# Optimization experiments

Measured on AMD Instinct MI355X. Metric: run time of the kernel, lower is better.

The kernel has to match this reference:

```python
import jax, jax.numpy as jnp
import numpy as np

B, N, C = 4, 4096, 128  # batch, tokens (flattened 3D volume), channels
F = 128  # filters


def setup_inputs() -> dict:
    key = jax.random.key(0)
    ks = jax.random.split(key, 7)
    s = 1.0 / np.sqrt(C)
    return {
        "inputs": jax.random.normal(ks[0], (B, N, C), dtype=jnp.float32),
        "Wq": jax.random.normal(ks[1], (C, F), dtype=jnp.float32) * s,
        "bq": jnp.zeros((F,), dtype=jnp.float32),
        "Wk": jax.random.normal(ks[2], (C, F), dtype=jnp.float32) * s,
        "bk": jnp.zeros((F,), dtype=jnp.float32),
        "Wv": jax.random.normal(ks[3], (C, F), dtype=jnp.float32) * s,
        "bv": jnp.zeros((F,), dtype=jnp.float32),
    }


def reference(inputs, Wq, bq, Wk, bk, Wv, bv):
    # Dense projections
    q = inputs @ Wq + bq  # [B, N, F]
    k = inputs @ Wk + bk
    v = inputs @ Wv + bv
    scale = jnp.sqrt(jnp.asarray(F, dtype=q.dtype))
    scores = jnp.einsum("bnf,bmf->bnm", q, k) / scale  # [B, N, N]
    weights = jax.nn.softmax(scores, axis=-1)
    return jnp.einsum("bnm,bmf->bnf", weights, v)
```

## Files before the change

### kernel.cpp

```cpp
#include <hip/hip_runtime.h>

typedef unsigned short u16;
typedef unsigned int u32;
typedef float f32x4 __attribute__((ext_vector_type(4)));
typedef short s16x8 __attribute__((ext_vector_type(8)));
typedef unsigned int u32x2 __attribute__((ext_vector_type(2)));
typedef unsigned int u32x4 __attribute__((ext_vector_type(4)));

#define NB 4
#define NT 4096
#define ND 128
#define NQ (NB * NT)

#define QK_SCALE 0.12751879523138906f

using as3_void = __attribute__((address_space(3))) void;
using as1_void = __attribute__((address_space(1))) void;

__device__ __forceinline__ u16 f2bf(float x){
  unsigned u = __float_as_uint(x);
  return (u16)((u + 0x7FFFu + ((u >> 16) & 1u)) >> 16);
}
__device__ __forceinline__ u32 cvtpk(float lo, float hi){
  u32 r; asm("v_cvt_pk_bf16_f32 %0, %1, %2" : "=v"(r) : "v"(lo), "v"(hi)); return r;
}
__device__ __forceinline__ f32x4 mfma16(s16x8 a, s16x8 b, f32x4 c){
  return __builtin_amdgcn_mfma_f32_16x16x32_bf16(a, b, c, 0, 0, 0);
}

__global__ void k_wprep(const float* __restrict__ Wq, const float* __restrict__ Wk,
                        const float* __restrict__ Wv, u16* __restrict__ WT){
  int mat = blockIdx.x >> 7;
  int f   = blockIdx.x & 127;
  const float* W = (mat == 0) ? Wq : (mat == 1) ? Wk : Wv;
  int c = threadIdx.x;
  WT[mat * 16384 + f * 128 + c] = f2bf(W[c * 128 + f]);
}

__global__ __launch_bounds__(256) void k_proj(
    const float* __restrict__ X, const u16* __restrict__ WT,
    const float* __restrict__ bq, const float* __restrict__ bk, const float* __restrict__ bv,
    u16* __restrict__ Qs, u16* __restrict__ Ks, u16* __restrict__ VTs)
{
  __shared__ u16 vt[128 * 64];
  const int lane = threadIdx.x & 63;
  const int w    = threadIdx.x >> 6;
  const int lm = lane & 15, lg = lane >> 4;
  const int L   = (blockIdx.x & 7) * 96 + (blockIdx.x >> 3);
  const int mat = L % 3;
  const int rb  = L / 3;
  const int rowbase = rb * 64 + w * 16;

  s16x8 a[4];
  const float* xr = X + (size_t)(rowbase + lm) * ND;
  #pragma unroll
  for (int kc = 0; kc < 4; ++kc){
    f32x4 x0 = *(const f32x4*)(xr + kc * 32 + lg * 8);
    f32x4 x1 = *(const f32x4*)(xr + kc * 32 + lg * 8 + 4);
    s16x8 t;
    t[0]=(short)f2bf(x0[0]); t[1]=(short)f2bf(x0[1]); t[2]=(short)f2bf(x0[2]); t[3]=(short)f2bf(x0[3]);
    t[4]=(short)f2bf(x1[0]); t[5]=(short)f2bf(x1[1]); t[6]=(short)f2bf(x1[2]); t[7]=(short)f2bf(x1[3]);
    a[kc] = t;
  }

  const float* bias = (mat == 0) ? bq : (mat == 1) ? bk : bv;
  float bl[8];
  #pragma unroll
  for (int n = 0; n < 8; ++n) bl[n] = bias[n * 16 + lm];
  f32x4 acc[8];
  #pragma unroll
  for (int n = 0; n < 8; ++n) acc[n] = f32x4{0.f,0.f,0.f,0.f};
  #pragma unroll
  for (int kc = 0; kc < 4; ++kc){
    #pragma unroll
    for (int n = 0; n < 8; ++n){
      s16x8 bf = *(const s16x8*)&WT[mat*16384 + (n*16 + lm)*128 + kc*32 + lg*8];
      acc[n] = mfma16(a[kc], bf, acc[n]);
    }
  }

  if (mat == 0){
    #pragma unroll
    for (int n = 0; n < 8; ++n){
      int f = n * 16 + lm;
      #pragma unroll
      for (int i = 0; i < 4; ++i){
        int r = rowbase + lg * 4 + i;
        Qs[(size_t)r * ND + f] = f2bf((acc[n][i] + bl[n]) * QK_SCALE);
      }
    }
  } else if (mat == 1){
    #pragma unroll
    for (int n = 0; n < 8; ++n){
      int f = n * 16 + lm;
      #pragma unroll
      for (int i = 0; i < 4; ++i){
        int r = rowbase + lg * 4 + i;
        Ks[(size_t)r * ND + (f ^ ((r & 7) << 3))] = f2bf(acc[n][i] + bl[n]);
      }
    }
  } else {
    #pragma unroll
    for (int n = 0; n < 8; ++n){
      int f = n * 16 + lm;
      #pragma unroll
      for (int i = 0; i < 4; ++i){
        int stcol = (w * 16 + lg * 4 + i) ^ ((f & 3) << 3) ^ (((f >> 2) & 1) << 2);
        vt[f * 64 + (stcol ^ ((f & 7) << 3))] = f2bf(acc[n][i] + bl[n]);
      }
    }
    __syncthreads();
    const int b2  = (rb * 64) >> 12;
    const int nt0 = (rb * 64) & (NT - 1);
    #pragma unroll
    for (int it = 0; it < 4; ++it){
      int c = it * 256 + threadIdx.x;
      int f = c >> 3, ch = c & 7;
      s16x8 v = *(const s16x8*)&vt[f * 64 + ((ch * 8) ^ ((f & 7) << 3))];
      *(s16x8*)&VTs[((size_t)b2 * ND + f) * NT + nt0 + ch * 8] = v;
    }
  }
}

__global__ __launch_bounds__(256, 4) void k_attn(
    const u16* __restrict__ Qs, const u16* __restrict__ Ks,
    const u16* __restrict__ VTs, u16* __restrict__ Op, float* __restrict__ lp)
{
  __shared__ __align__(16) u16 kbuf[2][32 * 128];
  __shared__ __align__(16) u16 vbuf[2][128 * 32];

  const int lin = blockIdx.x;
  const int qblk   = (lin & 7) * 16 + (lin >> 6);
  const int eighth = (lin >> 3) & 7;

  const int lane = threadIdx.x & 63;
  const int qw = threadIdx.x >> 6;
  const int lm = lane & 15, lg = lane >> 4;
  const int q0 = qblk * 128 + qw * 32;
  const int b  = q0 >> 12;
  const int kv0 = eighth * 512;

  s16x8 aq[2][4];
  #pragma unroll
  for (int sq = 0; sq < 2; ++sq){
    const u16* qr = Qs + (size_t)(q0 + sq * 16 + lm) * ND;
    #pragma unroll
    for (int kc = 0; kc < 4; ++kc) aq[sq][kc] = *(const s16x8*)(qr + kc * 32 + lg * 8);
  }

  f32x4 o[2][8];
  #pragma unroll
  for (int sq = 0; sq < 2; ++sq)
    #pragma unroll
    for (int n = 0; n < 8; ++n) o[sq][n] = f32x4{0.f,0.f,0.f,0.f};
  float l_[2] = {0.f, 0.f};

  const u16* gk = Ks  + ((size_t)b * NT + kv0 + qw * 8 + (lane >> 4)) * ND + (lane & 15) * 8;
  const u16* gv = VTs + ((size_t)b * ND + qw * 32 + (lane >> 2)) * NT + kv0 + (lane & 3) * 8;

  auto stage = [&](int buf){
    u16* kd = &kbuf[buf][qw * 1024];
    u16* vd = &vbuf[buf][qw * 1024];
    __builtin_amdgcn_global_load_lds((const as1_void*)gk,
                                     (as3_void*)kd, 16, 0, 0);
    __builtin_amdgcn_global_load_lds((const as1_void*)(gk + (size_t)4 * ND),
                                     (as3_void*)(kd + 512), 16, 0, 0);
    __builtin_amdgcn_global_load_lds((const as1_void*)gv,
                                     (as3_void*)vd, 16, 0, 0);
    __builtin_amdgcn_global_load_lds((const as1_void*)(gv + (size_t)16 * NT),
                                     (as3_void*)(vd + 512), 16, 0, 0);
    gk += (size_t)32 * ND;
    gv += 32;
  };

  const int kswz = (lm & 7) << 3;
  const int vswz = ((lm & 3) << 3) ^ (((lm >> 2) & 1) << 2);
  const int vcol0 = (lg * 4) ^ vswz;
  const int vcol1 = (16 + lg * 4) ^ vswz;

  stage(0);
  __syncthreads();
  int par = 0;

  for (int t = 0; t < 16; ++t){
    if (t < 15) stage(par ^ 1);
    const u16* kb = &kbuf[par][0];
    const u16* vb = &vbuf[par][0];

    f32x4 st[2][2];
    #pragma unroll
    for (int sq = 0; sq < 2; ++sq)
      #pragma unroll
      for (int n = 0; n < 2; ++n) st[sq][n] = f32x4{0.f,0.f,0.f,0.f};
    __builtin_amdgcn_s_setprio(1);
    #pragma unroll
    for (int kc = 0; kc < 4; ++kc){
      #pragma unroll
      for (int n = 0; n < 2; ++n){
        s16x8 kf = *(const s16x8*)&kb[(n * 16 + lm) * 128 + ((kc * 32 + lg * 8) ^ kswz)];
        st[0][n] = mfma16(kf, aq[0][kc], st[0][n]);
        st[1][n] = mfma16(kf, aq[1][kc], st[1][n]);
      }
    }
    __builtin_amdgcn_s_setprio(0);

    s16x8 pa[2];
    #pragma unroll
    for (int sq = 0; sq < 2; ++sq){
      float p[8];
      #pragma unroll
      for (int n = 0; n < 2; ++n)
        #pragma unroll
        for (int i = 0; i < 4; ++i){
          p[n * 4 + i] = __builtin_amdgcn_exp2f(st[sq][n][i]);
          l_[sq] += p[n * 4 + i];
        }
      pa[sq] = __builtin_bit_cast(s16x8, u32x4{
          cvtpk(p[0], p[1]), cvtpk(p[2], p[3]),
          cvtpk(p[4], p[5]), cvtpk(p[6], p[7])});
    }

    __builtin_amdgcn_s_setprio(1);
    #pragma unroll
    for (int nf = 0; nf < 8; ++nf){
      const int vr = (nf * 16 + lm) * 32;
      u32x2 v0 = *(const u32x2*)&vb[vr + vcol0];
      u32x2 v1 = *(const u32x2*)&vb[vr + vcol1];
      s16x8 vf = __builtin_bit_cast(s16x8, u32x4{v0[0], v0[1], v1[0], v1[1]});
      o[0][nf] = mfma16(pa[0], vf, o[0][nf]);
      o[1][nf] = mfma16(pa[1], vf, o[1][nf]);
    }
    __builtin_amdgcn_s_setprio(0);

    __syncthreads();
    par ^= 1;
  }

  #pragma unroll
  for (int sq = 0; sq < 2; ++sq){
    float v = l_[sq];
    v += __shfl_xor(v, 16);
    v += __shfl_xor(v, 32);
    l_[sq] = v;
  }
  #pragma unroll
  for (int sq = 0; sq < 2; ++sq){
    #pragma unroll
    for (int i = 0; i < 4; ++i){
      const size_t r = (size_t)eighth * NQ + q0 + sq * 16 + lg * 4 + i;
      #pragma unroll
      for (int nf = 0; nf < 8; ++nf)
        Op[r * ND + nf * 16 + lm] = f2bf(o[sq][nf][i]);
    }
    if (lg == 0) lp[(size_t)eighth * NQ + q0 + sq * 16 + lm] = l_[sq];
  }
}

__global__ __launch_bounds__(256) void k_merge(const u16* __restrict__ Op,
                                               const float* __restrict__ lp,
                                               float* __restrict__ Out){
  const int gid = blockIdx.x * 256 + threadIdx.x;
  const int q = gid >> 4, c = gid & 15;
  float lsum = 0.f;
  #pragma unroll
  for (int e = 0; e < 8; ++e) lsum += lp[(size_t)e * NQ + q];
  const float inv = 1.f / lsum;
  float acc[8] = {0,0,0,0,0,0,0,0};
  #pragma unroll
  for (int e = 0; e < 8; ++e){
    s16x8 v = *(const s16x8*)(Op + ((size_t)e * NQ + q) * ND + c * 8);
    #pragma unroll
    for (int j = 0; j < 8; ++j)
      acc[j] += __uint_as_float(((u32)(u16)v[j]) << 16);
  }
  f32x4 r0{acc[0]*inv, acc[1]*inv, acc[2]*inv, acc[3]*inv};
  f32x4 r1{acc[4]*inv, acc[5]*inv, acc[6]*inv, acc[7]*inv};
  *(f32x4*)(Out + (size_t)q * ND + c * 8)     = r0;
  *(f32x4*)(Out + (size_t)q * ND + c * 8 + 4) = r1;
}

extern "C" void kernel_launch(void* const* d_in, const int* in_sizes, int n_in,
                              void* d_out, int out_size, void* d_ws, size_t ws_size,
                              hipStream_t stream) {
  const float* X  = (const float*)d_in[0];
  const float* Wq = (const float*)d_in[1];
  const float* bq = (const float*)d_in[2];
  const float* Wk = (const float*)d_in[3];
  const float* bk = (const float*)d_in[4];
  const float* Wv = (const float*)d_in[5];
  const float* bv = (const float*)d_in[6];
  float* Out = (float*)d_out;

  u16* Qs  = (u16*)d_ws;
  u16* Ks  = Qs  + (size_t)NQ * ND;
  u16* VTs = Ks  + (size_t)NQ * ND;
  u16* WT  = VTs + (size_t)NQ * ND;
  u16* Op  = WT + 3 * 128 * 128;
  float* lp = (float*)(Op + (size_t)8 * NQ * ND);

  hipLaunchKernelGGL(k_wprep, dim3(3 * 128), dim3(128), 0, stream, Wq, Wk, Wv, WT);
  hipLaunchKernelGGL(k_proj,  dim3(768), dim3(256), 0, stream,
                     X, WT, bq, bk, bv, Qs, Ks, VTs);
  hipLaunchKernelGGL(k_attn,  dim3(1024), dim3(256), 0, stream, Qs, Ks, VTs, Op, lp);
  hipLaunchKernelGGL(k_merge, dim3(NQ * 16 / 256), dim3(256), 0, stream, Op, lp, Out);
}
```

Baseline: 81.87 us.

## Triple-buffer K/V staging with split loads and explicit waitcnt barriers

Replaces the double-buffered K/V LDS pipeline in the attention kernel with a three-stage ring. K and V tiles are now issued separately, two tiles ahead, and each wait uses explicit vmcnt/lgkmcnt counters with raw s_barrier instead of __syncthreads. K and V fragments are loaded into registers before each MFMA phase so LDS reads are grouped away from the matrix ops. This costs 50% more LDS and a lower launch-bounds occupancy hint (3 instead of 4), and adds more barriers per iteration.

```diff
diff --git a/kernel.cpp b/kernel.cpp
--- a/kernel.cpp
+++ b/kernel.cpp
@@ -122,12 +122,12 @@
   }
 }
 
-__global__ __launch_bounds__(256, 4) void k_attn(
+__global__ __launch_bounds__(256, 3) void k_attn(
     const u16* __restrict__ Qs, const u16* __restrict__ Ks,
     const u16* __restrict__ VTs, u16* __restrict__ Op, float* __restrict__ lp)
 {
-  __shared__ __align__(16) u16 kbuf[2][32 * 128];
-  __shared__ __align__(16) u16 vbuf[2][128 * 32];
+  __shared__ __align__(16) u16 kbuf[3][32 * 128];
+  __shared__ __align__(16) u16 vbuf[3][128 * 32];
 
   const int lin = blockIdx.x;
   const int qblk   = (lin & 7) * 16 + (lin >> 6);
@@ -158,18 +158,18 @@
   const u16* gk = Ks  + ((size_t)b * NT + kv0 + qw * 8 + (lane >> 4)) * ND + (lane & 15) * 8;
   const u16* gv = VTs + ((size_t)b * ND + qw * 32 + (lane >> 2)) * NT + kv0 + (lane & 3) * 8;
 
-  auto stage = [&](int buf){
+  auto stageK = [&](int buf){
     u16* kd = &kbuf[buf][qw * 1024];
-    u16* vd = &vbuf[buf][qw * 1024];
-    __builtin_amdgcn_global_load_lds((const as1_void*)gk,
-                                     (as3_void*)kd, 16, 0, 0);
+    __builtin_amdgcn_global_load_lds((const as1_void*)gk, (as3_void*)kd, 16, 0, 0);
     __builtin_amdgcn_global_load_lds((const as1_void*)(gk + (size_t)4 * ND),
                                      (as3_void*)(kd + 512), 16, 0, 0);
-    __builtin_amdgcn_global_load_lds((const as1_void*)gv,
-                                     (as3_void*)vd, 16, 0, 0);
+    gk += (size_t)32 * ND;
+  };
+  auto stageV = [&](int buf){
+    u16* vd = &vbuf[buf][qw * 1024];
+    __builtin_amdgcn_global_load_lds((const as1_void*)gv, (as3_void*)vd, 16, 0, 0);
     __builtin_amdgcn_global_load_lds((const as1_void*)(gv + (size_t)16 * NT),
                                      (as3_void*)(vd + 512), 16, 0, 0);
-    gk += (size_t)32 * ND;
     gv += 32;
   };
 
@@ -178,15 +178,30 @@
   const int vcol0 = (lg * 4) ^ vswz;
   const int vcol1 = (16 + lg * 4) ^ vswz;
 
-  stage(0);
-  __syncthreads();
-  int par = 0;
+  stageK(0); stageV(0); stageK(1); stageV(1);
+
+  int r = 0, s = 2;
 
   for (int t = 0; t < 16; ++t){
-    if (t < 15) stage(par ^ 1);
-    const u16* kb = &kbuf[par][0];
-    const u16* vb = &vbuf[par][0];
-
+    if (t < 15) asm volatile("s_waitcnt vmcnt(4)" ::: "memory");
+    else        asm volatile("s_waitcnt vmcnt(0)" ::: "memory");
+    __builtin_amdgcn_sched_barrier(0);
+    __builtin_amdgcn_s_barrier();
+    __builtin_amdgcn_sched_barrier(0);
+
+    const u16* kb = &kbuf[r][0];
+    const u16* vb = &vbuf[r][0];
+
+    s16x8 kf[2][4];
+    #pragma unroll
+    for (int kc = 0; kc < 4; ++kc){
+      kf[0][kc] = *(const s16x8*)&kb[lm * 128        + ((kc * 32 + lg * 8) ^ kswz)];
+      kf[1][kc] = *(const s16x8*)&kb[(16 + lm) * 128 + ((kc * 32 + lg * 8) ^ kswz)];
+    }
+    if (t < 14) stageK(s);
+    __builtin_amdgcn_s_barrier();
+    asm volatile("s_waitcnt lgkmcnt(0)" ::: "memory");
+    __builtin_amdgcn_sched_barrier(0);
     f32x4 st[2][2];
     #pragma unroll
     for (int sq = 0; sq < 2; ++sq)
@@ -197,12 +212,12 @@
     for (int kc = 0; kc < 4; ++kc){
       #pragma unroll
       for (int n = 0; n < 2; ++n){
-        s16x8 kf = *(const s16x8*)&kb[(n * 16 + lm) * 128 + ((kc * 32 + lg * 8) ^ kswz)];
-        st[0][n] = mfma16(kf, aq[0][kc], st[0][n]);
-        st[1][n] = mfma16(kf, aq[1][kc], st[1][n]);
+        st[0][n] = mfma16(kf[n][kc], aq[0][kc], st[0][n]);
+        st[1][n] = mfma16(kf[n][kc], aq[1][kc], st[1][n]);
       }
     }
     __builtin_amdgcn_s_setprio(0);
+    __builtin_amdgcn_s_barrier();
 
     s16x8 pa[2];
     #pragma unroll
@@ -219,21 +234,29 @@
           cvtpk(p[0], p[1]), cvtpk(p[2], p[3]),
           cvtpk(p[4], p[5]), cvtpk(p[6], p[7])});
     }
-
-    __builtin_amdgcn_s_setprio(1);
+    if (t < 14) stageV(s);
+    s16x8 vf[8];
     #pragma unroll
     for (int nf = 0; nf < 8; ++nf){
       const int vr = (nf * 16 + lm) * 32;
       u32x2 v0 = *(const u32x2*)&vb[vr + vcol0];
       u32x2 v1 = *(const u32x2*)&vb[vr + vcol1];
-      s16x8 vf = __builtin_bit_cast(s16x8, u32x4{v0[0], v0[1], v1[0], v1[1]});
-      o[0][nf] = mfma16(pa[0], vf, o[0][nf]);
-      o[1][nf] = mfma16(pa[1], vf, o[1][nf]);
+      vf[nf] = __builtin_bit_cast(s16x8, u32x4{v0[0], v0[1], v1[0], v1[1]});
+    }
+    __builtin_amdgcn_s_barrier();
+    asm volatile("s_waitcnt lgkmcnt(0)" ::: "memory");
+    __builtin_amdgcn_sched_barrier(0);
+    __builtin_amdgcn_s_setprio(1);
+    #pragma unroll
+    for (int nf = 0; nf < 8; ++nf){
+      o[0][nf] = mfma16(pa[0], vf[nf], o[0][nf]);
+      o[1][nf] = mfma16(pa[1], vf[nf], o[1][nf]);
     }
     __builtin_amdgcn_s_setprio(0);
-
-    __syncthreads();
-    par ^= 1;
+    __builtin_amdgcn_s_barrier();
+
+    r = (r == 2) ? 0 : r + 1;
+    s = (s == 2) ? 0 : s + 1;
   }
 
   #pragma unroll
@@ -247,10 +270,10 @@
   for (int sq = 0; sq < 2; ++sq){
     #pragma unroll
     for (int i = 0; i < 4; ++i){
-      const size_t r = (size_t)eighth * NQ + q0 + sq * 16 + lg * 4 + i;
+      const size_t rr = (size_t)eighth * NQ + q0 + sq * 16 + lg * 4 + i;
       #pragma unroll
       for (int nf = 0; nf < 8; ++nf)
-        Op[r * ND + nf * 16 + lm] = f2bf(o[sq][nf][i]);
+        Op[rr * ND + nf * 16 + lm] = f2bf(o[sq][nf][i]);
     }
     if (lg == 0) lp[(size_t)eighth * NQ + q0 + sq * 16 + lm] = l_[sq];
   }
```

Measured after the change: 81.19 us. Within noise of the previous version (-0.8%).
